# Kernel tuning notes

Measured on AMD Instinct MI355X. Metric: run time of the kernel, lower is better.

The kernel has to match this reference:

```python
import jax, jax.numpy as jnp
import numpy as np

N = 512          # octave output grid resolution per cube side
M = 256          # input octave resolution
FACTOR = 0.5     # 2 ** (-factor), factor = 1
EPS = 1e-12


def make_cube_faces(n):
    # two triangles per quad on each of the 6 n x n side grids
    idx = np.arange(n * n).reshape(n, n)
    a = idx[:-1, :-1].ravel(); b = idx[:-1, 1:].ravel()
    c = idx[1:, :-1].ravel(); d = idx[1:, 1:].ravel()
    tris = np.concatenate([np.stack([a, b, c], 1), np.stack([b, d, c], 1)], 0)
    faces = np.concatenate([tris + s * n * n for s in range(6)], 0)
    return jnp.asarray(faces, jnp.int32)  # [F, 3]


def to_stacked(t):
    # [1, 6*m*m, 3] -> [6, 3, m, m]
    m = int(round((t.shape[1] // 6) ** 0.5))
    return t.reshape(6, m, m, 3).transpose(0, 3, 1, 2)


def to_vertices(s):
    # [6, 3, m, m] -> [1, 6*m*m, 3]
    return s.transpose(0, 2, 3, 1).reshape(1, -1, 3)


def resize_bilinear_ac(t, n):
    # bilinear, align_corners=True, square input [.., m, m] -> [.., n, n]
    m = t.shape[-1]
    coords = jnp.linspace(0.0, m - 1.0, n)
    i0 = jnp.clip(jnp.floor(coords).astype(jnp.int32), 0, m - 1)
    i1 = jnp.minimum(i0 + 1, m - 1)
    w = (coords - i0).astype(t.dtype)
    t = t[..., i0, :] * (1.0 - w)[:, None] + t[..., i1, :] * w[:, None]
    t = t[..., :, i0] * (1.0 - w) + t[..., :, i1] * w
    return t


def compute_face_normals(vert, faces):
    v = vert[0]                                  # [V, 3]
    v0, v1, v2 = v[faces[:, 0]], v[faces[:, 1]], v[faces[:, 2]]
    fn = jnp.cross(v1 - v0, v2 - v0)             # [F, 3]
    nrm = jnp.linalg.norm(fn, axis=-1, keepdims=True)
    return fn / jnp.maximum(nrm, EPS)


def compute_vertex_normals(vert, faces, face_normals):
    V = vert.shape[1]
    flat_idx = faces.reshape(-1)                          # [3F] f0v0,f0v1,f0v2,...
    rep = jnp.repeat(face_normals, 3, axis=0)             # [3F, 3]
    acc = jax.ops.segment_sum(rep, flat_idx, num_segments=V)  # scatter-add
    nrm = jnp.linalg.norm(acc, axis=-1, keepdims=True)
    return (acc / jnp.maximum(nrm, EPS))[None]            # [1, V, 3]


def get_vertex_normals(vert, faces):
    fn = compute_face_normals(vert, faces)
    normals = compute_vertex_normals(vert, faces, fn)
    stacked = to_stacked(normals)                         # [6, 3, n, n]
    sign = jnp.array([-1.0, 1.0, 1.0, -1.0, -1.0, 1.0], stacked.dtype)
    stacked = stacked * sign[:, None, None, None]
    return to_vertices(stacked)


def setup_inputs() -> dict:
    key = jax.random.key(0)
    k1, k2 = jax.random.split(key)
    vrt = jax.random.normal(k1, (1, 6 * M * M, 3), jnp.float32)
    nrm = jax.random.normal(k2, (1, 6 * M * M, 3), jnp.float32)
    ps = jnp.zeros((6, 1, N, N), jnp.float32)   # nn.Parameter(zeros * noise)
    faces = make_cube_faces(N)
    return {"vrt": vrt, "nrm": nrm, "ps": ps, "faces": faces}


def reference(vrt, nrm, ps, faces):
    vrt_s = resize_bilinear_ac(to_stacked(vrt), N)                 # [6,3,n,n]
    nrm_mag = jnp.linalg.norm(resize_bilinear_ac(to_stacked(nrm), N),
                              axis=1, keepdims=True)               # [6,1,n,n]
    stacked = vrt_s + FACTOR * jax.nn.sigmoid(ps) * nrm_mag
    vert = to_vertices(stacked)                                    # [1, V, 3]
    normals = get_vertex_normals(vert, faces)
    return vert, faces, normals
```

## Files before the change

### kernel.cpp

```cpp
#include <hip/hip_runtime.h>
#include <math.h>

#define NSZ 512
#define MSZ 256
#define NPIX (6 * NSZ * NSZ)
#define NQu  261121u
#define NQ2u 522242u
#define NFACE 3133452
#define F3TOT 9400356
#define NFT12 783363
#define TS 32
#define HS 34
#define QS 33
#define NVB 1536
#define NFB ((NFT12 + 255) / 256)
#define GRID (NVB + NFB)

typedef __fp16 h2_t __attribute__((ext_vector_type(2)));

__device__ inline float fast_rcp(float x) {
    float r = __builtin_amdgcn_rcpf(x);
    return r * (2.0f - x * r);
}
__device__ inline float fast_rsqrt(float d) {
    float r = __builtin_amdgcn_rsqf(d);
    return r * (1.5f - 0.5f * d * r * r);
}
__device__ inline float fast_sigmoid(float x) {
    float e = __builtin_amdgcn_exp2f(-1.442695040888963f * x);
    return fast_rcp(1.0f + e);
}
__device__ inline float lerpf(float a, float b, float w) {
    return __builtin_fmaf(w, b - a, a);
}
__device__ inline unsigned pkh2(float x, float y) {
    h2_t h = __builtin_amdgcn_cvt_pkrtz(x, y);
    return __builtin_bit_cast(unsigned, h);
}
__device__ inline float2 uph2(unsigned u) {
    h2_t h = __builtin_bit_cast(h2_t, u);
    return make_float2((float)h.x, (float)h.y);
}

__global__ __launch_bounds__(256) void k_all(const float* __restrict__ vrt,
                                             const float* __restrict__ nrm,
                                             const float* __restrict__ ps,
                                             float* __restrict__ out0,
                                             float* __restrict__ out1,
                                             float* __restrict__ out2) {
    __shared__ float sv [HS * HS * 3];
    __shared__ uint2 tn0p[QS * QS];
    __shared__ uint2 tn1p[QS * QS];

    int blk = blockIdx.x;

    if (blk >= NVB) {
        int t = (blk - NVB) * 256 + threadIdx.x;
        if (t >= NFT12) return;
        unsigned tri = 4u * (unsigned)t;
        unsigned s   = tri / NQ2u;
        unsigned r1  = tri - s * NQ2u;
        unsigned ty  = (r1 >= NQu) ? 1u : 0u;
        unsigned qi  = r1 - ty * NQu;
        unsigned R   = qi / 511u;
        unsigned Q   = qi - R * 511u;

        unsigned a[4], tt[4];
        unsigned aq = Q, aR = R, aty = ty, as_ = s;
#pragma unroll
        for (int k = 0; k < 4; ++k) {
            a[k]  = (as_ << 18) + (aR << 9) + aq;
            tt[k] = aty;
            aq++;
            if (aq == 511u) {
                aq = 0u; aR++;
                if (aR == 511u) { aR = 0u; aty ^= 1u; if (aty == 0u) as_++; }
            }
        }
        float w[12];
#pragma unroll
        for (int k = 0; k < 4; ++k) {
            w[3*k + 0] = (float)(a[k] + (tt[k] ? 1u : 0u));
            w[3*k + 1] = (float)(a[k] + (tt[k] ? 513u : 1u));
            w[3*k + 2] = (float)(a[k] + 512u);
        }
        float4* o = (float4*)out1 + 3 * t;
        o[0] = make_float4(w[0], w[1], w[2],  w[3]);
        o[1] = make_float4(w[4], w[5], w[6],  w[7]);
        o[2] = make_float4(w[8], w[9], w[10], w[11]);
        return;
    }

    int f   = blk >> 8;
    int tl  = blk & 255;
    int tr  = (tl >> 4) * TS;
    int tq  = (tl & 15) * TS;
    int fbm = f * (MSZ * MSZ);
    int fbn = f * (NSZ * NSZ);

    const float scale = 255.0f / 511.0f;
    for (int p = threadIdx.x; p < HS * HS; p += 256) {
        int pr = p / HS, pq = p - pr * HS;
        int y = tr + pr - 1, x = tq + pq - 1;
        int yc = min(max(y, 0), NSZ - 1);
        int xc = min(max(x, 0), NSZ - 1);

        float cy = (float)yc * scale;
        float cx = (float)xc * scale;
        int iy0 = min((int)cy, MSZ - 1);
        int ix0 = min((int)cx, MSZ - 1);
        float wy = cy - (float)iy0;
        float wx = cx - (float)ix0;
        int   iya = min(iy0, MSZ - 2);
        int   ixa = min(ix0, MSZ - 2);
        float wya = (iy0 < MSZ - 1) ? wy : 1.0f;
        float wxa = (ix0 < MSZ - 1) ? wx : 1.0f;

        int g0 = (fbm + iya * MSZ + ixa) * 3;
        int g1 = g0 + MSZ * 3;

        float va0 = vrt[g0], va1 = vrt[g0+1], va2 = vrt[g0+2];
        float va3 = vrt[g0+3], va4 = vrt[g0+4], va5 = vrt[g0+5];
        float vb0 = vrt[g1], vb1 = vrt[g1+1], vb2 = vrt[g1+2];
        float vb3 = vrt[g1+3], vb4 = vrt[g1+4], vb5 = vrt[g1+5];
        float vx = lerpf(lerpf(va0, va3, wxa), lerpf(vb0, vb3, wxa), wya);
        float vy = lerpf(lerpf(va1, va4, wxa), lerpf(vb1, vb4, wxa), wya);
        float vz = lerpf(lerpf(va2, va5, wxa), lerpf(vb2, vb5, wxa), wya);

        float na0 = nrm[g0], na1 = nrm[g0+1], na2 = nrm[g0+2];
        float na3 = nrm[g0+3], na4 = nrm[g0+4], na5 = nrm[g0+5];
        float nb0 = nrm[g1], nb1 = nrm[g1+1], nb2 = nrm[g1+2];
        float nb3 = nrm[g1+3], nb4 = nrm[g1+4], nb5 = nrm[g1+5];
        float nx = lerpf(lerpf(na0, na3, wxa), lerpf(nb0, nb3, wxa), wya);
        float ny = lerpf(lerpf(na1, na4, wxa), lerpf(nb1, nb4, wxa), wya);
        float nz = lerpf(lerpf(na2, na5, wxa), lerpf(nb2, nb5, wxa), wya);

        float mag = __builtin_amdgcn_sqrtf(nx * nx + ny * ny + nz * nz);
        float sig = fast_sigmoid(ps[fbn + yc * NSZ + xc]);
        float add = 0.5f * sig * mag;
        float ox = vx + add, oy = vy + add, oz = vz + add;

        sv[p * 3 + 0] = ox;
        sv[p * 3 + 1] = oy;
        sv[p * 3 + 2] = oz;
        if (pr >= 1 && pr <= TS && pq >= 1 && pq <= TS) {
            int gi = (fbn + y * NSZ + x) * 3;
            out0[gi + 0] = ox;
            out0[gi + 1] = oy;
            out0[gi + 2] = oz;
        }
    }
    __syncthreads();

    for (int p = threadIdx.x; p < QS * QS; p += 256) {
        int Ri = p / QS, Qi = p - Ri * QS;
        int base = (Ri * HS + Qi) * 3;
        float Axx = sv[base + 0],        Axy = sv[base + 1],        Axz = sv[base + 2];
        float Bxx = sv[base + 3],        Bxy = sv[base + 4],        Bxz = sv[base + 5];
        float Cxx = sv[base + HS*3 + 0], Cxy = sv[base + HS*3 + 1], Cxz = sv[base + HS*3 + 2];
        float Dxx = sv[base + HS*3 + 3], Dxy = sv[base + HS*3 + 4], Dxz = sv[base + HS*3 + 5];

        {
            float e1x = Bxx - Axx, e1y = Bxy - Axy, e1z = Bxz - Axz;
            float e2x = Cxx - Axx, e2y = Cxy - Axy, e2z = Cxz - Axz;
            float nx = e1y * e2z - e1z * e2y;
            float ny = e1z * e2x - e1x * e2z;
            float nz = e1x * e2y - e1y * e2x;
            float d  = fmaxf(nx * nx + ny * ny + nz * nz, 1e-24f);
            float r  = fast_rsqrt(d);
            tn0p[p] = make_uint2(pkh2(nx * r, ny * r), pkh2(nz * r, 0.0f));
        }
        {
            float e1x = Dxx - Bxx, e1y = Dxy - Bxy, e1z = Dxz - Bxz;
            float e2x = Cxx - Bxx, e2y = Cxy - Bxy, e2z = Cxz - Bxz;
            float nx = e1y * e2z - e1z * e2y;
            float ny = e1z * e2x - e1x * e2z;
            float nz = e1x * e2y - e1y * e2x;
            float d  = fmaxf(nx * nx + ny * ny + nz * nz, 1e-24f);
            float r  = fast_rsqrt(d);
            tn1p[p] = make_uint2(pkh2(nx * r, ny * r), pkh2(nz * r, 0.0f));
        }
    }
    __syncthreads();

    float sg = (f == 1 || f == 2 || f == 5) ? 1.0f : -1.0f;
    for (int p = threadIdx.x; p < TS * TS; p += 256) {
        int r = p >> 5, q = p & 31;
        int q00 = r * QS + q;
        int q01 = q00 + 1;
        int q10 = q00 + QS;
        int q11 = q10 + 1;

        uint2 u0 = tn0p[q11], u1 = tn0p[q10], u2 = tn0p[q01];
        uint2 u3 = tn1p[q10], u4 = tn1p[q00], u5 = tn1p[q01];

        float2 p0 = uph2(u0.x), p1 = uph2(u1.x), p2 = uph2(u2.x);
        float2 p3 = uph2(u3.x), p4 = uph2(u4.x), p5 = uph2(u5.x);
        float2 z0 = uph2(u0.y), z1 = uph2(u1.y), z2 = uph2(u2.y);
        float2 z3 = uph2(u3.y), z4 = uph2(u4.y), z5 = uph2(u5.y);

        float ax = p0.x + p1.x + p2.x + p3.x + p4.x + p5.x;
        float ay = p0.y + p1.y + p2.y + p3.y + p4.y + p5.y;
        float az = z0.x + z1.x + z2.x + z3.x + z4.x + z5.x;

        float d  = fmaxf(ax * ax + ay * ay + az * az, 1e-24f);
        float rs = fast_rsqrt(d) * sg;
        int gi = (fbn + (tr + r) * NSZ + (tq + q)) * 3;
        out2[gi + 0] = ax * rs;
        out2[gi + 1] = ay * rs;
        out2[gi + 2] = az * rs;
    }
}

extern "C" void kernel_launch(void* const* d_in, const int* in_sizes, int n_in,
                              void* d_out, int out_size, void* d_ws, size_t ws_size,
                              hipStream_t stream) {
    const float* vrt = (const float*)d_in[0];
    const float* nrm = (const float*)d_in[1];
    const float* ps  = (const float*)d_in[2];

    float* out0 = (float*)d_out;
    float* out1 = out0 + (size_t)NPIX * 3;
    float* out2 = out1 + (size_t)F3TOT;

    k_all<<<GRID, 256, 0, stream>>>(vrt, nrm, ps, out0, out1, out2);
}
```

Baseline: 26.47 us.

## Stage tile vertices in fp16 and repack normal LDS arrays to raise occupancy

The interpolated vertex tile is now stored in shared memory as packed fp16 (xy in one word, z in a short) instead of three fp32 values. Face normals are stored as separate xy arrays plus a shared z-pair word instead of padded uint2 entries. Together these cut LDS use per block, and launch bounds now request 8 blocks per CU to raise occupancy and LDS bandwidth headroom. The trade-off is lower precision: computing cross products from fp16-rounded vertex positions can hurt the accuracy of the normals.

Measured after the change: 26.84 us. No clear change (+1.4%).

```diff
diff --git a/kernel.cpp b/kernel.cpp
--- a/kernel.cpp
+++ b/kernel.cpp
@@ -41,16 +41,22 @@
     h2_t h = __builtin_bit_cast(h2_t, u);
     return make_float2((float)h.x, (float)h.y);
 }
-
-__global__ __launch_bounds__(256) void k_all(const float* __restrict__ vrt,
-                                             const float* __restrict__ nrm,
-                                             const float* __restrict__ ps,
-                                             float* __restrict__ out0,
-                                             float* __restrict__ out1,
-                                             float* __restrict__ out2) {
-    __shared__ float sv [HS * HS * 3];
-    __shared__ uint2 tn0p[QS * QS];
-    __shared__ uint2 tn1p[QS * QS];
+__device__ inline float uph_lo(unsigned u) {
+    h2_t h = __builtin_bit_cast(h2_t, u);
+    return (float)h.x;
+}
+
+__global__ __launch_bounds__(256, 8) void k_all(const float* __restrict__ vrt,
+                                                const float* __restrict__ nrm,
+                                                const float* __restrict__ ps,
+                                                float* __restrict__ out0,
+                                                float* __restrict__ out1,
+                                                float* __restrict__ out2) {
+    __shared__ unsigned svXY[HS * HS];
+    __shared__ unsigned short svZ[HS * HS];
+    __shared__ unsigned tnXY0[QS * QS];
+    __shared__ unsigned tnXY1[QS * QS];
+    __shared__ unsigned tnZZ [QS * QS];
 
     int blk = blockIdx.x;
 
@@ -119,30 +125,34 @@
         int g0 = (fbm + iya * MSZ + ixa) * 3;
         int g1 = g0 + MSZ * 3;
 
-        float va0 = vrt[g0], va1 = vrt[g0+1], va2 = vrt[g0+2];
-        float va3 = vrt[g0+3], va4 = vrt[g0+4], va5 = vrt[g0+5];
-        float vb0 = vrt[g1], vb1 = vrt[g1+1], vb2 = vrt[g1+2];
-        float vb3 = vrt[g1+3], vb4 = vrt[g1+4], vb5 = vrt[g1+5];
-        float vx = lerpf(lerpf(va0, va3, wxa), lerpf(vb0, vb3, wxa), wya);
-        float vy = lerpf(lerpf(va1, va4, wxa), lerpf(vb1, vb4, wxa), wya);
-        float vz = lerpf(lerpf(va2, va5, wxa), lerpf(vb2, vb5, wxa), wya);
-
-        float na0 = nrm[g0], na1 = nrm[g0+1], na2 = nrm[g0+2];
-        float na3 = nrm[g0+3], na4 = nrm[g0+4], na5 = nrm[g0+5];
-        float nb0 = nrm[g1], nb1 = nrm[g1+1], nb2 = nrm[g1+2];
-        float nb3 = nrm[g1+3], nb4 = nrm[g1+4], nb5 = nrm[g1+5];
-        float nx = lerpf(lerpf(na0, na3, wxa), lerpf(nb0, nb3, wxa), wya);
-        float ny = lerpf(lerpf(na1, na4, wxa), lerpf(nb1, nb4, wxa), wya);
-        float nz = lerpf(lerpf(na2, na5, wxa), lerpf(nb2, nb5, wxa), wya);
+        float vx, vy, vz;
+        {
+            float a0 = vrt[g0], a1 = vrt[g0+1], a2 = vrt[g0+2];
+            float a3 = vrt[g0+3], a4 = vrt[g0+4], a5 = vrt[g0+5];
+            float b0 = vrt[g1], b1 = vrt[g1+1], b2 = vrt[g1+2];
+            float b3 = vrt[g1+3], b4 = vrt[g1+4], b5 = vrt[g1+5];
+            vx = lerpf(lerpf(a0, a3, wxa), lerpf(b0, b3, wxa), wya);
+            vy = lerpf(lerpf(a1, a4, wxa), lerpf(b1, b4, wxa), wya);
+            vz = lerpf(lerpf(a2, a5, wxa), lerpf(b2, b5, wxa), wya);
+        }
+        float nx, ny, nz;
+        {
+            float a0 = nrm[g0], a1 = nrm[g0+1], a2 = nrm[g0+2];
+            float a3 = nrm[g0+3], a4 = nrm[g0+4], a5 = nrm[g0+5];
+            float b0 = nrm[g1], b1 = nrm[g1+1], b2 = nrm[g1+2];
+            float b3 = nrm[g1+3], b4 = nrm[g1+4], b5 = nrm[g1+5];
+            nx = lerpf(lerpf(a0, a3, wxa), lerpf(b0, b3, wxa), wya);
+            ny = lerpf(lerpf(a1, a4, wxa), lerpf(b1, b4, wxa), wya);
+            nz = lerpf(lerpf(a2, a5, wxa), lerpf(b2, b5, wxa), wya);
+        }
 
         float mag = __builtin_amdgcn_sqrtf(nx * nx + ny * ny + nz * nz);
         float sig = fast_sigmoid(ps[fbn + yc * NSZ + xc]);
         float add = 0.5f * sig * mag;
         float ox = vx + add, oy = vy + add, oz = vz + add;
 
-        sv[p * 3 + 0] = ox;
-        sv[p * 3 + 1] = oy;
-        sv[p * 3 + 2] = oz;
+        svXY[p] = pkh2(ox, oy);
+        svZ[p]  = (unsigned short)(pkh2(oz, 0.0f) & 0xffffu);
         if (pr >= 1 && pr <= TS && pq >= 1 && pq <= TS) {
             int gi = (fbn + y * NSZ + x) * 3;
             out0[gi + 0] = ox;
@@ -154,32 +164,41 @@
 
     for (int p = threadIdx.x; p < QS * QS; p += 256) {
         int Ri = p / QS, Qi = p - Ri * QS;
-        int base = (Ri * HS + Qi) * 3;
-        float Axx = sv[base + 0],        Axy = sv[base + 1],        Axz = sv[base + 2];
-        float Bxx = sv[base + 3],        Bxy = sv[base + 4],        Bxz = sv[base + 5];
-        float Cxx = sv[base + HS*3 + 0], Cxy = sv[base + HS*3 + 1], Cxz = sv[base + HS*3 + 2];
-        float Dxx = sv[base + HS*3 + 3], Dxy = sv[base + HS*3 + 4], Dxz = sv[base + HS*3 + 5];
-
-        {
-            float e1x = Bxx - Axx, e1y = Bxy - Axy, e1z = Bxz - Axz;
-            float e2x = Cxx - Axx, e2y = Cxy - Axy, e2z = Cxz - Axz;
-            float nx = e1y * e2z - e1z * e2y;
-            float ny = e1z * e2x - e1x * e2z;
-            float nz = e1x * e2y - e1y * e2x;
-            float d  = fmaxf(nx * nx + ny * ny + nz * nz, 1e-24f);
+        int iA = Ri * HS + Qi;
+        int iB = iA + 1;
+        int iC = iA + HS;
+        int iD = iC + 1;
+
+        float2 Axy = uph2(svXY[iA]); float Az = uph_lo((unsigned)svZ[iA]);
+        float2 Bxy = uph2(svXY[iB]); float Bz = uph_lo((unsigned)svZ[iB]);
+        float2 Cxy = uph2(svXY[iC]); float Cz = uph_lo((unsigned)svZ[iC]);
+        float2 Dxy = uph2(svXY[iD]); float Dz = uph_lo((unsigned)svZ[iD]);
+
+        float n0x, n0y, n0z;
+        {
+            float e1x = Bxy.x - Axy.x, e1y = Bxy.y - Axy.y, e1z = Bz - Az;
+            float e2x = Cxy.x - Axy.x, e2y = Cxy.y - Axy.y, e2z = Cz - Az;
+            float cx = e1y * e2z - e1z * e2y;
+            float cy = e1z * e2x - e1x * e2z;
+            float cz = e1x * e2y - e1y * e2x;
+            float d  = fmaxf(cx * cx + cy * cy + cz * cz, 1e-24f);
             float r  = fast_rsqrt(d);
-            tn0p[p] = make_uint2(pkh2(nx * r, ny * r), pkh2(nz * r, 0.0f));
-        }
-        {
-            float e1x = Dxx - Bxx, e1y = Dxy - Bxy, e1z = Dxz - Bxz;
-            float e2x = Cxx - Bxx, e2y = Cxy - Bxy, e2z = Cxz - Bxz;
-            float nx = e1y * e2z - e1z * e2y;
-            float ny = e1z * e2x - e1x * e2z;
-            float nz = e1x * e2y - e1y * e2x;
-            float d  = fmaxf(nx * nx + ny * ny + nz * nz, 1e-24f);
+            n0x = cx * r; n0y = cy * r; n0z = cz * r;
+        }
+        float n1x, n1y, n1z;
+        {
+            float e1x = Dxy.x - Bxy.x, e1y = Dxy.y - Bxy.y, e1z = Dz - Bz;
+            float e2x = Cxy.x - Bxy.x, e2y = Cxy.y - Bxy.y, e2z = Cz - Bz;
+            float cx = e1y * e2z - e1z * e2y;
+            float cy = e1z * e2x - e1x * e2z;
+            float cz = e1x * e2y - e1y * e2x;
+            float d  = fmaxf(cx * cx + cy * cy + cz * cz, 1e-24f);
             float r  = fast_rsqrt(d);
-            tn1p[p] = make_uint2(pkh2(nx * r, ny * r), pkh2(nz * r, 0.0f));
-        }
+            n1x = cx * r; n1y = cy * r; n1z = cz * r;
+        }
+        tnXY0[p] = pkh2(n0x, n0y);
+        tnXY1[p] = pkh2(n1x, n1y);
+        tnZZ [p] = pkh2(n0z, n1z);
     }
     __syncthreads();
 
@@ -191,17 +210,20 @@
         int q10 = q00 + QS;
         int q11 = q10 + 1;
 
-        uint2 u0 = tn0p[q11], u1 = tn0p[q10], u2 = tn0p[q01];
-        uint2 u3 = tn1p[q10], u4 = tn1p[q00], u5 = tn1p[q01];
-
-        float2 p0 = uph2(u0.x), p1 = uph2(u1.x), p2 = uph2(u2.x);
-        float2 p3 = uph2(u3.x), p4 = uph2(u4.x), p5 = uph2(u5.x);
-        float2 z0 = uph2(u0.y), z1 = uph2(u1.y), z2 = uph2(u2.y);
-        float2 z3 = uph2(u3.y), z4 = uph2(u4.y), z5 = uph2(u5.y);
-
-        float ax = p0.x + p1.x + p2.x + p3.x + p4.x + p5.x;
-        float ay = p0.y + p1.y + p2.y + p3.y + p4.y + p5.y;
-        float az = z0.x + z1.x + z2.x + z3.x + z4.x + z5.x;
+        float2 a0 = uph2(tnXY0[q11]);
+        float2 a1 = uph2(tnXY0[q10]);
+        float2 a2 = uph2(tnXY0[q01]);
+        float2 b0 = uph2(tnXY1[q10]);
+        float2 b1 = uph2(tnXY1[q00]);
+        float2 b2 = uph2(tnXY1[q01]);
+        float2 zA = uph2(tnZZ[q11]);
+        float2 zB = uph2(tnZZ[q10]);
+        float2 zC = uph2(tnZZ[q01]);
+        float2 zD = uph2(tnZZ[q00]);
+
+        float ax = a0.x + a1.x + a2.x + b0.x + b1.x + b2.x;
+        float ay = a0.y + a1.y + a2.y + b0.y + b1.y + b2.y;
+        float az = zA.x + zB.x + zC.x + zB.y + zD.y + zC.y;
 
         float d  = fmaxf(ax * ax + ay * ay + az * az, 1e-24f);
         float rs = fast_rsqrt(d) * sg;
```
